# Performance work log

Hardware: AMD Instinct MI355X
Metric: run time of the kernel (lower is better)

Reference implementation:

```python
import jax, jax.numpy as jnp
import numpy as np

BLOCK_SIZE = 3
SOBEL_PAD = 1  # sobel_size // 2
BLOCK_PAD = BLOCK_SIZE // 2

_SOBEL_X = jnp.array([[-1.0, 0.0, 1.0], [-2.0, 0.0, 2.0], [-1.0, 0.0, 1.0]], dtype=jnp.float32)[None, None]
_SOBEL_Y = jnp.array([[-1.0, -2.0, -1.0], [0.0, 0.0, 0.0], [1.0, 2.0, 1.0]], dtype=jnp.float32)[None, None]
_SUM_K = jnp.ones((1, 1, BLOCK_SIZE, BLOCK_SIZE), dtype=jnp.float32)


def _pad_replicate(x, p):
    return jnp.pad(x, ((0, 0), (0, 0), (p, p), (p, p)), mode='edge')


def _conv(x, k):
    return jax.lax.conv_general_dilated(
        x, k, window_strides=(1, 1), padding='VALID',
        dimension_numbers=('NCHW', 'OIHW', 'NCHW'))


def setup_inputs() -> dict:
    key = jax.random.key(0)
    image = jax.random.uniform(key, (8, 1, 1080, 1920), dtype=jnp.float32) * 255.0
    return {"image": image}


def reference(image) -> jnp.ndarray:
    img = image.astype(jnp.float32)
    img_p = _pad_replicate(img, SOBEL_PAD)
    Ix = _conv(img_p, _SOBEL_X)
    Iy = _conv(img_p, _SOBEL_Y)
    Ixx = Ix * Ix
    Iyy = Iy * Iy
    Ixy = Ix * Iy
    sum_Ixx = _conv(_pad_replicate(Ixx, BLOCK_PAD), _SUM_K)
    sum_Iyy = _conv(_pad_replicate(Iyy, BLOCK_PAD), _SUM_K)
    sum_Ixy = _conv(_pad_replicate(Ixy, BLOCK_PAD), _SUM_K)
    half_trace = (sum_Ixx + sum_Iyy) * 0.5
    diff_half = (sum_Ixx - sum_Iyy) * 0.5
    sqrt_disc = jnp.sqrt(diff_half * diff_half + sum_Ixy * sum_Ixy + 1e-10)
    lambda_min = half_trace - sqrt_disc
    return jnp.clip(lambda_min, 0.0)
```

## Files before the change

kernel.cpp:

```cpp
#include <hip/hip_runtime.h>

#define IMG_H 1080
#define IMG_W 1920
#define NBATCH 8
#define TW 256
#define TH 24
#define SROWS (TH + 4)
#define SCOLS (TW + 4)
#define STRIP 6

__global__ __launch_bounds__(256, 4)
void shi_tomasi_kernel(const float* __restrict__ img, float* __restrict__ out) {
    __shared__ float S[SROWS * SCOLS];
    const int x0 = blockIdx.x * TW;
    const int y0 = blockIdx.y * TH;
    const int b  = blockIdx.z;
    const float* g = img + (size_t)b * (IMG_H * IMG_W);

    if (x0 >= 2 && x0 + SCOLS - 2 <= IMG_W) {
        for (int q = threadIdx.x; q < SROWS * 64; q += 256) {
            const int row = q >> 6, lane = q & 63;
            int gr = y0 + row - 2; gr = max(0, min(IMG_H - 1, gr));
            const float* src = g + (size_t)gr * IMG_W + (x0 + 4 * lane);
            const float4 v = *(const float4*)src;
            float* d = S + row * SCOLS + 2 + 4 * lane;
            ((float2*)d)[0] = make_float2(v.x, v.y);
            ((float2*)d)[1] = make_float2(v.z, v.w);
        }
        if (threadIdx.x < SROWS * 4) {
            const int row = threadIdx.x >> 2, e = threadIdx.x & 3;
            const int j = (e < 2) ? e : (TW + e);
            int gr = y0 + row - 2; gr = max(0, min(IMG_H - 1, gr));
            const int gc = x0 + j - 2;
            S[row * SCOLS + j] = g[(size_t)gr * IMG_W + gc];
        }
    } else {
        for (int p = threadIdx.x; p < SROWS * SCOLS; p += 256) {
            const int row = p / SCOLS;
            const int col = p - row * SCOLS;
            int gr = y0 + row - 2; gr = max(0, min(IMG_H - 1, gr));
            int gc = x0 + col - 2; gc = max(0, min(IMG_W - 1, gc));
            S[row * SCOLS + col] = g[(size_t)gr * IMG_W + gc];
        }
    }
    __syncthreads();

    const int tx = threadIdx.x & 63;
    const int ty = threadIdx.x >> 6;
    const int vb = x0 + 4 * tx;
    if (vb >= IMG_W) return;
    const int s0 = ty * STRIP;
    const bool fixL = (vb == 0);
    const bool fixR = (vb == IMG_W - 4);

    float* orow = out + ((size_t)b * IMG_H + (y0 + s0)) * IMG_W + vb;

    float h[3][12];

    #pragma unroll
    for (int rr = 0; rr < STRIP + 2; ++rr) {
        const int r = s0 - 1 + rr;
        int pr = y0 + r; pr = max(0, min(IMG_H - 1, pr));
        const int im = max(0, pr - 1) - y0 + 2;
        const int i0 = pr - y0 + 2;
        const int ip = min(IMG_H - 1, pr + 1) - y0 + 2;

        const float4* Rm = (const float4*)(S + im * SCOLS);
        const float4* R0 = (const float4*)(S + i0 * SCOLS);
        const float4* Rp = (const float4*)(S + ip * SCOLS);
        const float4 mA = Rm[tx], mB = Rm[tx + 1];
        const float4 zA = R0[tx], zB = R0[tx + 1];
        const float4 pA = Rp[tx], pB = Rp[tx + 1];
        const float m[8] = {mA.x, mA.y, mA.z, mA.w, mB.x, mB.y, mB.z, mB.w};
        const float z[8] = {zA.x, zA.y, zA.z, zA.w, zB.x, zB.y, zB.z, zB.w};
        const float p[8] = {pA.x, pA.y, pA.z, pA.w, pB.x, pB.y, pB.z, pB.w};

        float A[8], Bv[8];
        #pragma unroll
        for (int s = 0; s < 8; ++s) {
            A[s]  = m[s] + 2.0f * z[s] + p[s];
            Bv[s] = p[s] - m[s];
        }
        float Ix[6], Iy[6];
        #pragma unroll
        for (int s = 0; s < 6; ++s) {
            Ix[s] = A[s + 2] - A[s];
            Iy[s] = Bv[s] + 2.0f * Bv[s + 1] + Bv[s + 2];
        }
        if (fixL) { Ix[0] = A[3] - A[2]; Iy[0] = 3.0f * Bv[2] + Bv[3]; }
        if (fixR) { Ix[5] = A[5] - A[4]; Iy[5] = Bv[4] + 3.0f * Bv[5]; }

        float pxx[6], pyy[6], pxy[6];
        #pragma unroll
        for (int s = 0; s < 6; ++s) {
            pxx[s] = Ix[s] * Ix[s];
            pyy[s] = Iy[s] * Iy[s];
            pxy[s] = Ix[s] * Iy[s];
        }
        float* hr = h[rr % 3];
        #pragma unroll
        for (int o = 0; o < 4; ++o) {
            hr[o]     = pxx[o] + pxx[o + 1] + pxx[o + 2];
            hr[4 + o] = pyy[o] + pyy[o + 1] + pyy[o + 2];
            hr[8 + o] = pxy[o] + pxy[o + 1] + pxy[o + 2];
        }
        if (rr >= 2) {
            const float* h0 = h[(rr - 2) % 3];
            const float* h1 = h[(rr - 1) % 3];
            float rv[4];
            #pragma unroll
            for (int o = 0; o < 4; ++o) {
                const float sxx = h0[o]     + h1[o]     + hr[o];
                const float syy = h0[4 + o] + h1[4 + o] + hr[4 + o];
                const float sxy = h0[8 + o] + h1[8 + o] + hr[8 + o];
                const float ht   = 0.5f * (sxx + syy);
                const float dh   = 0.5f * (sxx - syy);
                const float disc = dh * dh + sxy * sxy + 1e-10f;
                const float lam  = ht - sqrtf(disc);
                rv[o] = fmaxf(lam, 0.0f);
            }
            *(float4*)orow = make_float4(rv[0], rv[1], rv[2], rv[3]);
            orow += IMG_W;
        }
    }
}

extern "C" void kernel_launch(void* const* d_in, const int* in_sizes, int n_in,
                              void* d_out, int out_size, void* d_ws, size_t ws_size,
                              hipStream_t stream) {
    const float* img = (const float*)d_in[0];
    float* out = (float*)d_out;
    dim3 grid((IMG_W + TW - 1) / TW, IMG_H / TH, NBATCH);
    shi_tomasi_kernel<<<grid, 256, 0, stream>>>(img, out);
}
```

Measured before the change: 132.3 us.

## Replace shared-memory tile with direct global row loads and separable rolling filters

The shared-memory staging and __syncthreads are removed. Each thread now reads its 8-wide image row window straight from global memory and keeps the horizontal Sobel partials (difference and smoothing) in a three-row register ring, so each input row is loaded and filtered horizontally only once per strip. Strips become 9 rows tall on a 128x72 block tile. Border replication is handled with explicit top, bottom, left and right fixups, and the discriminant now uses fmaf. This trades shared-memory traffic and the barrier for more global/L2 reads of overlapping halo columns and higher register pressure.

```diff
diff --git a/kernel.cpp b/kernel.cpp
--- a/kernel.cpp
+++ b/kernel.cpp
@@ -3,121 +3,101 @@
 #define IMG_H 1080
 #define IMG_W 1920
 #define NBATCH 8
-#define TW 256
-#define TH 24
-#define SROWS (TH + 4)
-#define SCOLS (TW + 4)
-#define STRIP 6
 
 __global__ __launch_bounds__(256, 4)
 void shi_tomasi_kernel(const float* __restrict__ img, float* __restrict__ out) {
-    __shared__ float S[SROWS * SCOLS];
-    const int x0 = blockIdx.x * TW;
-    const int y0 = blockIdx.y * TH;
+    const int cg    = threadIdx.x & 31;
+    const int strip = threadIdx.x >> 5;
+    const int vb = blockIdx.x * 128 + cg * 4;
+    const int s0 = blockIdx.y * 72 + strip * 9;
     const int b  = blockIdx.z;
     const float* g = img + (size_t)b * (IMG_H * IMG_W);
 
-    if (x0 >= 2 && x0 + SCOLS - 2 <= IMG_W) {
-        for (int q = threadIdx.x; q < SROWS * 64; q += 256) {
-            const int row = q >> 6, lane = q & 63;
-            int gr = y0 + row - 2; gr = max(0, min(IMG_H - 1, gr));
-            const float* src = g + (size_t)gr * IMG_W + (x0 + 4 * lane);
-            const float4 v = *(const float4*)src;
-            float* d = S + row * SCOLS + 2 + 4 * lane;
-            ((float2*)d)[0] = make_float2(v.x, v.y);
-            ((float2*)d)[1] = make_float2(v.z, v.w);
-        }
-        if (threadIdx.x < SROWS * 4) {
-            const int row = threadIdx.x >> 2, e = threadIdx.x & 3;
-            const int j = (e < 2) ? e : (TW + e);
-            int gr = y0 + row - 2; gr = max(0, min(IMG_H - 1, gr));
-            const int gc = x0 + j - 2;
-            S[row * SCOLS + j] = g[(size_t)gr * IMG_W + gc];
-        }
-    } else {
-        for (int p = threadIdx.x; p < SROWS * SCOLS; p += 256) {
-            const int row = p / SCOLS;
-            const int col = p - row * SCOLS;
-            int gr = y0 + row - 2; gr = max(0, min(IMG_H - 1, gr));
-            int gc = x0 + col - 2; gc = max(0, min(IMG_W - 1, gc));
-            S[row * SCOLS + col] = g[(size_t)gr * IMG_W + gc];
-        }
-    }
-    __syncthreads();
+    const bool eL = (vb == 0);
+    const bool eR = (vb == IMG_W - 4);
+    const int  o0 = eL ? 0 : (eR ? vb - 4 : vb - 2);
+    const bool topFix = (s0 == 0);
+    const bool botFix = (s0 + 9 == IMG_H);
 
-    const int tx = threadIdx.x & 63;
-    const int ty = threadIdx.x >> 6;
-    const int vb = x0 + 4 * tx;
-    if (vb >= IMG_W) return;
-    const int s0 = ty * STRIP;
-    const bool fixL = (vb == 0);
-    const bool fixR = (vb == IMG_W - 4);
+    float hdR[3][6], hsR[3][6], hfd[3], hfs[3], h[3][12];
 
-    float* orow = out + ((size_t)b * IMG_H + (y0 + s0)) * IMG_W + vb;
+    auto load_row = [&](int lr, float* hd, float* hs, float& fd, float& fs) {
+        const float* rp = g + (size_t)lr * IMG_W + o0;
+        const float2 p0 = *(const float2*)(rp);
+        const float2 p1 = *(const float2*)(rp + 2);
+        const float2 p2 = *(const float2*)(rp + 4);
+        const float2 p3 = *(const float2*)(rp + 6);
+        float z0=p0.x, z1=p0.y, z2=p1.x, z3=p1.y, z4=p2.x, z5=p2.y, z6=p3.x, z7=p3.y;
+        if (eL) { z7=z5; z6=z4; z5=z3; z4=z2; z3=z1; z2=z0; z1=z0; }
+        if (eR) { z0=z2; z1=z3; z2=z4; z3=z5; z4=z6; z5=z7; z6=z7; }
+        hd[0]=z2-z0; hd[1]=z3-z1; hd[2]=z4-z2; hd[3]=z5-z3; hd[4]=z6-z4; hd[5]=z7-z5;
+        hs[0]=z0+2.0f*z1+z2; hs[1]=z1+2.0f*z2+z3; hs[2]=z2+2.0f*z3+z4;
+        hs[3]=z3+2.0f*z4+z5; hs[4]=z4+2.0f*z5+z6; hs[5]=z5+2.0f*z6+z7;
+        fd = eR ? (z5-z4) : (z3-z2);
+        fs = eR ? (z4+3.0f*z5) : (3.0f*z2+z3);
+    };
 
-    float h[3][12];
+    load_row(max(s0-2,0), hdR[0], hsR[0], hfd[0], hfs[0]);
+    load_row(max(s0-1,0), hdR[1], hsR[1], hfd[1], hfs[1]);
+
+    float* orow = out + ((size_t)b * IMG_H + s0) * IMG_W + vb;
 
     #pragma unroll
-    for (int rr = 0; rr < STRIP + 2; ++rr) {
-        const int r = s0 - 1 + rr;
-        int pr = y0 + r; pr = max(0, min(IMG_H - 1, pr));
-        const int im = max(0, pr - 1) - y0 + 2;
-        const int i0 = pr - y0 + 2;
-        const int ip = min(IMG_H - 1, pr + 1) - y0 + 2;
+    for (int rr = 0; rr < 11; ++rr) {
+        const int sm = rr % 3;
+        const int sz = (rr + 1) % 3;
+        const int sp = (rr + 2) % 3;
+        load_row(min(s0 + rr, IMG_H - 1), hdR[sp], hsR[sp], hfd[sp], hfs[sp]);
 
-        const float4* Rm = (const float4*)(S + im * SCOLS);
-        const float4* R0 = (const float4*)(S + i0 * SCOLS);
-        const float4* Rp = (const float4*)(S + ip * SCOLS);
-        const float4 mA = Rm[tx], mB = Rm[tx + 1];
-        const float4 zA = R0[tx], zB = R0[tx + 1];
-        const float4 pA = Rp[tx], pB = Rp[tx + 1];
-        const float m[8] = {mA.x, mA.y, mA.z, mA.w, mB.x, mB.y, mB.z, mB.w};
-        const float z[8] = {zA.x, zA.y, zA.z, zA.w, zB.x, zB.y, zB.z, zB.w};
-        const float p[8] = {pA.x, pA.y, pA.z, pA.w, pB.x, pB.y, pB.z, pB.w};
-
-        float A[8], Bv[8];
-        #pragma unroll
-        for (int s = 0; s < 8; ++s) {
-            A[s]  = m[s] + 2.0f * z[s] + p[s];
-            Bv[s] = p[s] - m[s];
-        }
         float Ix[6], Iy[6];
         #pragma unroll
-        for (int s = 0; s < 6; ++s) {
-            Ix[s] = A[s + 2] - A[s];
-            Iy[s] = Bv[s] + 2.0f * Bv[s + 1] + Bv[s + 2];
+        for (int t = 0; t < 6; ++t) {
+            Ix[t] = hdR[sm][t] + 2.0f * hdR[sz][t] + hdR[sp][t];
+            Iy[t] = hsR[sp][t] - hsR[sm][t];
         }
-        if (fixL) { Ix[0] = A[3] - A[2]; Iy[0] = 3.0f * Bv[2] + Bv[3]; }
-        if (fixR) { Ix[5] = A[5] - A[4]; Iy[5] = Bv[4] + 3.0f * Bv[5]; }
+        const float ixf = hfd[sm] + 2.0f * hfd[sz] + hfd[sp];
+        const float iyf = hfs[sp] - hfs[sm];
+        if (eL) { Ix[0] = ixf; Iy[0] = iyf; }
+        if (eR) { Ix[5] = ixf; Iy[5] = iyf; }
 
         float pxx[6], pyy[6], pxy[6];
         #pragma unroll
-        for (int s = 0; s < 6; ++s) {
-            pxx[s] = Ix[s] * Ix[s];
-            pyy[s] = Iy[s] * Iy[s];
-            pxy[s] = Ix[s] * Iy[s];
+        for (int t = 0; t < 6; ++t) {
+            pxx[t] = Ix[t] * Ix[t];
+            pyy[t] = Iy[t] * Iy[t];
+            pxy[t] = Ix[t] * Iy[t];
         }
         float* hr = h[rr % 3];
         #pragma unroll
         for (int o = 0; o < 4; ++o) {
-            hr[o]     = pxx[o] + pxx[o + 1] + pxx[o + 2];
-            hr[4 + o] = pyy[o] + pyy[o + 1] + pyy[o + 2];
-            hr[8 + o] = pxy[o] + pxy[o + 1] + pxy[o + 2];
+            hr[o]     = pxx[o] + pxx[o+1] + pxx[o+2];
+            hr[4 + o] = pyy[o] + pyy[o+1] + pyy[o+2];
+            hr[8 + o] = pxy[o] + pxy[o+1] + pxy[o+2];
         }
+        if (rr == 1) {
+            #pragma unroll
+            for (int q = 0; q < 12; ++q) if (topFix) h[0][q] = hr[q];
+        }
+        if (rr == 10) {
+            const float* hprev = h[(rr - 1) % 3];
+            #pragma unroll
+            for (int q = 0; q < 12; ++q) if (botFix) hr[q] = hprev[q];
+        }
+
         if (rr >= 2) {
             const float* h0 = h[(rr - 2) % 3];
             const float* h1 = h[(rr - 1) % 3];
+            const float* h2 = h[rr % 3];
             float rv[4];
             #pragma unroll
             for (int o = 0; o < 4; ++o) {
-                const float sxx = h0[o]     + h1[o]     + hr[o];
-                const float syy = h0[4 + o] + h1[4 + o] + hr[4 + o];
-                const float sxy = h0[8 + o] + h1[8 + o] + hr[8 + o];
+                const float sxx = h0[o]     + h1[o]     + h2[o];
+                const float syy = h0[4 + o] + h1[4 + o] + h2[4 + o];
+                const float sxy = h0[8 + o] + h1[8 + o] + h2[8 + o];
                 const float ht   = 0.5f * (sxx + syy);
                 const float dh   = 0.5f * (sxx - syy);
-                const float disc = dh * dh + sxy * sxy + 1e-10f;
-                const float lam  = ht - sqrtf(disc);
-                rv[o] = fmaxf(lam, 0.0f);
+                const float disc = fmaf(dh, dh, fmaf(sxy, sxy, 1e-10f));
+                rv[o] = fmaxf(ht - sqrtf(disc), 0.0f);
             }
             *(float4*)orow = make_float4(rv[0], rv[1], rv[2], rv[3]);
             orow += IMG_W;
@@ -130,6 +110,6 @@
                               hipStream_t stream) {
     const float* img = (const float*)d_in[0];
     float* out = (float*)d_out;
-    dim3 grid((IMG_W + TW - 1) / TW, IMG_H / TH, NBATCH);
+    dim3 grid(IMG_W / 128, IMG_H / 72, NBATCH);
     shi_tomasi_kernel<<<grid, 256, 0, stream>>>(img, out);
 }
```

New measurement: 125.4 us. 5.2% less time.
